# Kernel optimization log

Hardware: AMD Instinct MI355X
Metric: run time of the kernel (lower is better)

The kernel has to match this reference:

```python
import jax, jax.numpy as jnp
import numpy as np

H = 16  # hidden_size
NUM_MLP = 8   # relu, tanh, elu, silu, gelu, none, selu, softplus
NUM_EXPERTS = 12  # 8 MLPs + abs, modulus, sin, cos


def setup_inputs() -> dict:
    key = jax.random.key(0)
    ks = jax.random.split(key, 6)
    B, S, C = 16, 2048, 16
    x = jax.random.normal(ks[0], (B, S, C, 2), dtype=jnp.float32)
    # Stacked per-expert MLP params: Linear(3 -> H) then Linear(H -> 1).
    # (Torch init zeroes the last layer; we use random weights to exercise the math.)
    W1 = jax.random.normal(ks[1], (NUM_MLP, 3, H), dtype=jnp.float32) * (1.0 / np.sqrt(3.0))
    b1 = jax.random.normal(ks[2], (NUM_MLP, H), dtype=jnp.float32) * 0.02
    W2 = jax.random.normal(ks[3], (NUM_MLP, H, 1), dtype=jnp.float32) * (1.0 / np.sqrt(H))
    b2 = jax.random.normal(ks[4], (NUM_MLP, 1), dtype=jnp.float32) * 0.02
    expert_weights = jnp.full((NUM_EXPERTS,), 1.0 / NUM_EXPERTS, dtype=jnp.float32)
    return {"x": x, "W1": W1, "b1": b1, "W2": W2, "b2": b2,
            "expert_weights": expert_weights}


_ACTS = [
    jax.nn.relu,
    jnp.tanh,
    jax.nn.elu,
    jax.nn.silu,
    lambda v: jax.nn.gelu(v, approximate=False),  # torch nn.GELU default = exact
    lambda v: v,                                   # 'none'
    jax.nn.selu,
    jax.nn.softplus,
]


def reference(x, W1, b1, W2, b2, expert_weights):
    # x: (B, S, C, 2) -> output (B, S, C, 1, 1)
    re, im = x[..., 0], x[..., 1]
    amp = jnp.sqrt(re * re + im * im)            # torch.norm over last dim
    feats = jnp.stack([re, im, amp], axis=-1)    # (B,S,C,3)

    outs = []
    for i, act in enumerate(_ACTS):
        h = act(feats @ W1[i] + b1[i])           # (B,S,C,H)
        outs.append(h @ W2[i] + b2[i])           # (B,S,C,1)

    outs.append((jnp.abs(re) + jnp.abs(im))[..., None])  # 'abs'
    outs.append(amp[..., None])                           # 'modulus'
    outs.append(jnp.sin(amp)[..., None])                  # 'sin'
    outs.append(jnp.cos(amp)[..., None])                  # 'cos'

    expert_outputs = jnp.stack(outs, axis=-1)    # (B,S,C,1,12)
    return jnp.sum(expert_outputs * expert_weights, axis=-1, keepdims=True)  # (B,S,C,1,1)
```

## Files before the change

kernel.cpp:

```cpp
#include <hip/hip_runtime.h>

constexpr int BLK = 256;

__device__ __forceinline__ float fast_rcp(float x) { return __builtin_amdgcn_rcpf(x); }

__device__ __forceinline__ float fast_exp2(float x) {
#if __has_builtin(__builtin_amdgcn_exp2f)
    return __builtin_amdgcn_exp2f(x);
#else
    return __expf(x * 0.6931471805599453f);
#endif
}

#define LOG2E 1.4426950408889634f

__device__ __forceinline__ float max0(float x) { return fmaxf(x, 0.0f); }
__device__ __forceinline__ float min0(float x) { return fminf(x, 0.0f); }

template<int A> __device__ __forceinline__ float act_fn(float z);
template<> __device__ __forceinline__ float act_fn<0>(float z) { return max0(z); }
template<> __device__ __forceinline__ float act_fn<1>(float z) {
    float e = fast_exp2(z * (2.0f * LOG2E));
    return fmaf(-2.0f, fast_rcp(e + 1.0f), 1.0f);
}
template<> __device__ __forceinline__ float act_fn<2>(float z) {
    float em = fast_exp2(z * LOG2E) - 1.0f;
    return max0(z) + min0(em);
}
template<> __device__ __forceinline__ float act_fn<3>(float z) {
    float d = fast_exp2(z * (-LOG2E)) + 1.0f;
    return z * fast_rcp(d);
}
template<> __device__ __forceinline__ float act_fn<4>(float z) {
    float d = fast_exp2(z * (-1.702f * LOG2E)) + 1.0f;
    return z * fast_rcp(d);
}
template<> __device__ __forceinline__ float act_fn<5>(float z) { return z; }
template<> __device__ __forceinline__ float act_fn<6>(float z) {
    const float sc   = 1.0507009873554805f;
    const float scal = 1.7580993408473766f;
    float e = fast_exp2(z * LOG2E);
    float n = fmaf(scal, e, -scal);
    return fmaf(max0(z), sc, min0(n));
}
template<> __device__ __forceinline__ float act_fn<7>(float z) {
    float m = fast_exp2(fabsf(z) * (-LOG2E)) + 1.0f;
    float p = fmaf(-0.056570851f, m, 0.44717955f);
    p = fmaf(p, m, -1.4699568f);
    p = fmaf(p, m, 2.8212026f);
    p = fmaf(p, m, -1.7417939f);
    return max0(z) + p;
}

template<int A>
__device__ __forceinline__ void run_expert(const float* __restrict__ W1,
                                           const float* __restrict__ b1,
                                           const float* __restrict__ W2,
                                           const float* __restrict__ ew,
                                           float re, float im, float am, float& acc) {
    float accE = 0.0f;
#pragma unroll
    for (int h = 0; h < 16; ++h) {
        const float wre = W1[A * 48 + h];
        const float wim = W1[A * 48 + 16 + h];
        const float wam = W1[A * 48 + 32 + h];
        const float bb  = b1[A * 16 + h];
        const float w2  = W2[A * 16 + h];
        float z = fmaf(re, wre, fmaf(im, wim, fmaf(am, wam, bb)));
        accE = fmaf(act_fn<A>(z), w2, accE);
    }
    acc = fmaf(accE, ew[A], acc);
    __builtin_amdgcn_sched_barrier(0);
}

__global__ __launch_bounds__(BLK, 8)
void moe_kernel(const float* __restrict__ x,
                const float* __restrict__ W1,
                const float* __restrict__ b1,
                const float* __restrict__ W2,
                const float* __restrict__ b2,
                const float* __restrict__ ew,
                float* __restrict__ out, int npts) {
    const int p = blockIdx.x * BLK + threadIdx.x;
    if (p >= npts) return;

    float bconst = 0.0f;
#pragma unroll
    for (int i = 0; i < 8; ++i) bconst = fmaf(ew[i], b2[i], bconst);

    float2 v = reinterpret_cast<const float2*>(x)[p];
    const float re = v.x, im = v.y;
    const float am = __builtin_amdgcn_sqrtf(fmaf(re, re, im * im));

    const float INV2PI = 0.15915494309189535f;
    const float s  = am * INV2PI;
    const float sn = __builtin_amdgcn_sinf(s);
    const float cs = __builtin_amdgcn_cosf(s);

    float acc = fmaf(ew[8], fabsf(re) + fabsf(im), bconst);
    acc = fmaf(ew[9],  am, acc);
    acc = fmaf(ew[10], sn, acc);
    acc = fmaf(ew[11], cs, acc);

    run_expert<0>(W1, b1, W2, ew, re, im, am, acc);
    run_expert<1>(W1, b1, W2, ew, re, im, am, acc);
    run_expert<2>(W1, b1, W2, ew, re, im, am, acc);
    run_expert<3>(W1, b1, W2, ew, re, im, am, acc);
    run_expert<4>(W1, b1, W2, ew, re, im, am, acc);
    run_expert<5>(W1, b1, W2, ew, re, im, am, acc);
    run_expert<6>(W1, b1, W2, ew, re, im, am, acc);
    run_expert<7>(W1, b1, W2, ew, re, im, am, acc);

    out[p] = acc;
}

extern "C" void kernel_launch(void* const* d_in, const int* in_sizes, int n_in,
                              void* d_out, int out_size, void* d_ws, size_t ws_size,
                              hipStream_t stream) {
    const float* x  = (const float*)d_in[0];
    const float* W1 = (const float*)d_in[1];
    const float* b1 = (const float*)d_in[2];
    const float* W2 = (const float*)d_in[3];
    const float* b2 = (const float*)d_in[4];
    const float* ew = (const float*)d_in[5];
    float* out = (float*)d_out;

    const int npts = in_sizes[0] / 2;
    const int blocks = (npts + BLK - 1) / BLK;
    hipLaunchKernelGGL(moe_kernel, dim3(blocks), dim3(BLK), 0, stream,
                       x, W1, b1, W2, b2, ew, out, npts);
}
```

Measured before the change: 24.44 us.

## Compute first MLP layer with bf16 MFMA and process two points per thread

```diff
diff --git a/kernel.cpp b/kernel.cpp
--- a/kernel.cpp
+++ b/kernel.cpp
@@ -1,21 +1,33 @@
 #include <hip/hip_runtime.h>
 
+typedef short  bf16x8 __attribute__((ext_vector_type(8)));
+typedef float  f32x16 __attribute__((ext_vector_type(16)));
+typedef unsigned int uint4v __attribute__((ext_vector_type(4)));
+
 constexpr int BLK = 256;
-
-__device__ __forceinline__ float fast_rcp(float x) { return __builtin_amdgcn_rcpf(x); }
-
-__device__ __forceinline__ float fast_exp2(float x) {
-#if __has_builtin(__builtin_amdgcn_exp2f)
-    return __builtin_amdgcn_exp2f(x);
-#else
-    return __expf(x * 0.6931471805599453f);
-#endif
-}
+constexpr int PTS_PER_BLOCK = 512;
 
 #define LOG2E 1.4426950408889634f
+#define LN2   0.6931471805599453f
 
+__device__ __forceinline__ float fast_rcp(float x)  { return __builtin_amdgcn_rcpf(x); }
+__device__ __forceinline__ float fast_exp2(float x) { return __builtin_amdgcn_exp2f(x); }
+__device__ __forceinline__ float fast_log2(float x) { return __builtin_amdgcn_logf(x); }
 __device__ __forceinline__ float max0(float x) { return fmaxf(x, 0.0f); }
 __device__ __forceinline__ float min0(float x) { return fminf(x, 0.0f); }
+
+__device__ __forceinline__ unsigned cvt_pk_bf16(float lo, float hi) {
+    unsigned r;
+    asm("v_cvt_pk_bf16_f32 %0, %1, %2" : "=v"(r) : "v"(lo), "v"(hi));
+    return r;
+}
+__device__ __forceinline__ float bperm_f(int src_lane, float v) {
+    int r = __builtin_amdgcn_ds_bpermute(src_lane << 2, __builtin_bit_cast(int, v));
+    return __builtin_bit_cast(float, r);
+}
+__device__ __forceinline__ unsigned bperm_u(int src_lane, unsigned v) {
+    return (unsigned)__builtin_amdgcn_ds_bpermute(src_lane << 2, (int)v);
+}
 
 template<int A> __device__ __forceinline__ float act_fn(float z);
 template<> __device__ __forceinline__ float act_fn<0>(float z) { return max0(z); }
@@ -28,7 +40,7 @@
     return max0(z) + min0(em);
 }
 template<> __device__ __forceinline__ float act_fn<3>(float z) {
-    float d = fast_exp2(z * (-LOG2E)) + 1.0f;
+    float d = fast_exp2(-z * LOG2E) + 1.0f;
     return z * fast_rcp(d);
 }
 template<> __device__ __forceinline__ float act_fn<4>(float z) {
@@ -37,43 +49,37 @@
 }
 template<> __device__ __forceinline__ float act_fn<5>(float z) { return z; }
 template<> __device__ __forceinline__ float act_fn<6>(float z) {
-    const float sc   = 1.0507009873554805f;
-    const float scal = 1.7580993408473766f;
+    const float sc = 1.0507009873554805f, scal = 1.7580993408473766f;
     float e = fast_exp2(z * LOG2E);
     float n = fmaf(scal, e, -scal);
     return fmaf(max0(z), sc, min0(n));
 }
 template<> __device__ __forceinline__ float act_fn<7>(float z) {
-    float m = fast_exp2(fabsf(z) * (-LOG2E)) + 1.0f;
-    float p = fmaf(-0.056570851f, m, 0.44717955f);
-    p = fmaf(p, m, -1.4699568f);
-    p = fmaf(p, m, 2.8212026f);
-    p = fmaf(p, m, -1.7417939f);
-    return max0(z) + p;
+    float d = fast_exp2(-fabsf(z) * LOG2E) + 1.0f;
+    return fmaf(LN2, fast_log2(d), max0(z));
 }
 
-template<int A>
-__device__ __forceinline__ void run_expert(const float* __restrict__ W1,
-                                           const float* __restrict__ b1,
-                                           const float* __restrict__ W2,
-                                           const float* __restrict__ ew,
-                                           float re, float im, float am, float& acc) {
-    float accE = 0.0f;
+template<int PAIR>
+__device__ __forceinline__ void process_pair(bf16x8 a, bf16x8 b0, bf16x8 b1,
+                                             const float (&w2)[16],
+                                             float& S0, float& S1) {
+    constexpr int E0 = PAIR * 2, E1 = PAIR * 2 + 1;
+    f32x16 zc = (f32x16)(0.0f);
+    f32x16 d0 = __builtin_amdgcn_mfma_f32_32x32x16_bf16(a, b0, zc, 0, 0, 0);
+    f32x16 d1 = __builtin_amdgcn_mfma_f32_32x32x16_bf16(a, b1, zc, 0, 0, 0);
 #pragma unroll
-    for (int h = 0; h < 16; ++h) {
-        const float wre = W1[A * 48 + h];
-        const float wim = W1[A * 48 + 16 + h];
-        const float wam = W1[A * 48 + 32 + h];
-        const float bb  = b1[A * 16 + h];
-        const float w2  = W2[A * 16 + h];
-        float z = fmaf(re, wre, fmaf(im, wim, fmaf(am, wam, bb)));
-        accE = fmaf(act_fn<A>(z), w2, accE);
+    for (int r = 0; r < 8; ++r) {
+        S0 = fmaf(act_fn<E0>(d0[r]), w2[r], S0);
+        S1 = fmaf(act_fn<E0>(d1[r]), w2[r], S1);
     }
-    acc = fmaf(accE, ew[A], acc);
-    __builtin_amdgcn_sched_barrier(0);
+#pragma unroll
+    for (int r = 8; r < 16; ++r) {
+        S0 = fmaf(act_fn<E1>(d0[r]), w2[r], S0);
+        S1 = fmaf(act_fn<E1>(d1[r]), w2[r], S1);
+    }
 }
 
-__global__ __launch_bounds__(BLK, 8)
+__global__ __launch_bounds__(BLK)
 void moe_kernel(const float* __restrict__ x,
                 const float* __restrict__ W1,
                 const float* __restrict__ b1,
@@ -81,37 +87,77 @@
                 const float* __restrict__ b2,
                 const float* __restrict__ ew,
                 float* __restrict__ out, int npts) {
-    const int p = blockIdx.x * BLK + threadIdx.x;
-    if (p >= npts) return;
+    const int lane = threadIdx.x & 63;
+    const int wid  = threadIdx.x >> 6;
+    const bool lo  = (lane < 32);
+
+    bf16x8 afrag[4];
+#pragma unroll
+    for (int pair = 0; pair < 4; ++pair) {
+        const int h  = lane & 31;
+        const int e  = pair * 2 + (h >> 4);
+        const int hh = h & 15;
+        const unsigned d0 = cvt_pk_bf16(W1[e * 48 + hh], W1[e * 48 + 16 + hh]);
+        const unsigned d1 = cvt_pk_bf16(W1[e * 48 + 32 + hh], b1[e * 16 + hh]);
+        uint4v u = { lo ? d0 : 0u, lo ? d1 : 0u, 0u, 0u };
+        afrag[pair] = __builtin_bit_cast(bf16x8, u);
+    }
+
+    const int hi4 = (lane >> 5) << 2;
+    float w2v[4][16];
+#pragma unroll
+    for (int pair = 0; pair < 4; ++pair) {
+#pragma unroll
+        for (int r = 0; r < 16; ++r) {
+            const int row = (r & 3) + 8 * (r >> 2) + hi4;
+            const int e   = pair * 2 + (row >> 4);
+            w2v[pair][r] = W2[e * 16 + (row & 15)] * ew[e];
+        }
+    }
 
     float bconst = 0.0f;
 #pragma unroll
     for (int i = 0; i < 8; ++i) bconst = fmaf(ew[i], b2[i], bconst);
+    const float ewA = ew[8], ewM = ew[9], ewS = ew[10], ewC = ew[11];
 
-    float2 v = reinterpret_cast<const float2*>(x)[p];
-    const float re = v.x, im = v.y;
-    const float am = __builtin_amdgcn_sqrtf(fmaf(re, re, im * im));
+#pragma unroll
+    for (int it = 0; it < 2; ++it) {
+        const int wavebase = (blockIdx.x * 4 + wid) * 128 + it * 64;
+        const int pt = wavebase + lane;
+        const bool ok = (pt < npts);
 
-    const float INV2PI = 0.15915494309189535f;
-    const float s  = am * INV2PI;
-    const float sn = __builtin_amdgcn_sinf(s);
-    const float cs = __builtin_amdgcn_cosf(s);
+        float2 v = ok ? reinterpret_cast<const float2*>(x)[pt] : make_float2(0.f, 0.f);
+        const float re = v.x, im = v.y;
+        const float am = __builtin_amdgcn_sqrtf(fmaf(re, re, im * im));
 
-    float acc = fmaf(ew[8], fabsf(re) + fabsf(im), bconst);
-    acc = fmaf(ew[9],  am, acc);
-    acc = fmaf(ew[10], sn, acc);
-    acc = fmaf(ew[11], cs, acc);
+        const float INV2PI = 0.15915494309189535f;
+        const float s  = am * INV2PI;
+        float acc_an = fmaf(ewA, fabsf(re) + fabsf(im), bconst);
+        acc_an = fmaf(ewM, am, acc_an);
+        acc_an = fmaf(ewS, __builtin_amdgcn_sinf(s), acc_an);
+        acc_an = fmaf(ewC, __builtin_amdgcn_cosf(s), acc_an);
 
-    run_expert<0>(W1, b1, W2, ew, re, im, am, acc);
-    run_expert<1>(W1, b1, W2, ew, re, im, am, acc);
-    run_expert<2>(W1, b1, W2, ew, re, im, am, acc);
-    run_expert<3>(W1, b1, W2, ew, re, im, am, acc);
-    run_expert<4>(W1, b1, W2, ew, re, im, am, acc);
-    run_expert<5>(W1, b1, W2, ew, re, im, am, acc);
-    run_expert<6>(W1, b1, W2, ew, re, im, am, acc);
-    run_expert<7>(W1, b1, W2, ew, re, im, am, acc);
+        const unsigned f0 = cvt_pk_bf16(re, im);
+        const unsigned f1 = cvt_pk_bf16(am, 1.0f);
+        uint4v b0u = { lo ? f0 : 0u, lo ? f1 : 0u, 0u, 0u };
+        bf16x8 bfrag0 = __builtin_bit_cast(bf16x8, b0u);
+        const unsigned f0s = bperm_u(lane ^ 32, f0);
+        const unsigned f1s = bperm_u(lane ^ 32, f1);
+        uint4v b1u = { lo ? f0s : 0u, lo ? f1s : 0u, 0u, 0u };
+        bf16x8 bfrag1 = __builtin_bit_cast(bf16x8, b1u);
 
-    out[p] = acc;
+        float S0 = 0.0f, S1 = 0.0f;
+        process_pair<0>(afrag[0], bfrag0, bfrag1, w2v[0], S0, S1);
+        process_pair<1>(afrag[1], bfrag0, bfrag1, w2v[1], S0, S1);
+        process_pair<2>(afrag[2], bfrag0, bfrag1, w2v[2], S0, S1);
+        process_pair<3>(afrag[3], bfrag0, bfrag1, w2v[3], S0, S1);
+
+        S0 += bperm_f(lane ^ 32, S0);
+        S1 += bperm_f(lane ^ 32, S1);
+
+        const float tot = (lo ? S0 : S1) + acc_an;
+        if (ok) out[pt] = tot;
+    }
 }
 
 extern "C" void kernel_launch(void* const* d_in, const int* in_sizes, int n_in,
@@ -126,7 +172,7 @@
     float* out = (float*)d_out;
 
     const int npts = in_sizes[0] / 2;
-    const int blocks = (npts + BLK - 1) / BLK;
+    const int blocks = (npts + PTS_PER_BLOCK - 1) / PTS_PER_BLOCK;
     hipLaunchKernelGGL(moe_kernel, dim3(blocks), dim3(BLK), 0, stream,
                        x, W1, b1, W2, b2, ew, out, npts);
 }
```

Result: faster. 22.67 us (-7.2%).
